# Kernel optimization log

Hardware: AMD Instinct MI355X
Metric: run time of the kernel (lower is better)

The kernel has to match this reference:

```python
import jax, jax.numpy as jnp
import numpy as np

B, T, X_DIM, Y_DIM, H_DIM = 16, 1000, 8, 4, 48
GAMMA = 1e-4
ITERS = 200


def setup_inputs() -> dict:
    key = jax.random.key(0)
    ks = jax.random.split(key, 20)
    def rn(i, shape, s=1.0):
        return jax.random.normal(ks[i], shape, dtype=jnp.float32) * jnp.float32(s)
    E = 2 * H_DIM + X_DIM  # edge-MLP input width = [h, h_nbr, message]
    s_e = float(1.0 / np.sqrt(E))
    s_h = float(1.0 / np.sqrt(H_DIM))
    A = rn(4, (X_DIM, X_DIM), 0.1)
    Bm = rn(5, (Y_DIM, Y_DIM), 0.1)
    z = lambda n: jnp.zeros((n,), jnp.float32)
    return dict(
        ys=rn(0, (B, T, Y_DIM)),
        hx0=rn(1, (B, H_DIM, T)),
        F_mat=jnp.eye(X_DIM, dtype=jnp.float32) + rn(2, (X_DIM, X_DIM), 0.05),
        H_mat=rn(3, (Y_DIM, X_DIM), 0.3),
        Q=A @ A.T + 0.5 * jnp.eye(X_DIM, dtype=jnp.float32),  # SPD process noise
        R=Bm @ Bm.T + 0.5 * jnp.eye(Y_DIM, dtype=jnp.float32),  # SPD obs noise
        W_hy=rn(6, (H_DIM, Y_DIM), 0.5), b_hy=z(H_DIM),
        W1_past=rn(7, (H_DIM, E), s_e), b1_past=z(H_DIM),
        W2_past=rn(8, (H_DIM, H_DIM), s_h), b2_past=z(H_DIM),
        W1_fut=rn(9, (H_DIM, E), s_e), b1_fut=z(H_DIM),
        W2_fut=rn(10, (H_DIM, H_DIM), s_h), b2_fut=z(H_DIM),
        W1_y=rn(11, (H_DIM, E), s_e), b1_y=z(H_DIM),
        W2_y=rn(12, (H_DIM, H_DIM), s_h), b2_y=z(H_DIM),
        W_ih=rn(13, (3 * H_DIM, H_DIM), s_h), b_ih=z(3 * H_DIM),
        W_hh=rn(14, (3 * H_DIM, H_DIM), s_h), b_hh=z(3 * H_DIM),
        W_dec=rn(15, (X_DIM, H_DIM), s_h), b_dec=z(X_DIM),
        iterations=ITERS,
    )


def reference(ys, hx0, F_mat, H_mat, Q, R, W_hy, b_hy,
              W1_past, b1_past, W2_past, b2_past,
              W1_fut, b1_fut, W2_fut, b2_fut,
              W1_y, b1_y, W2_y, b2_y,
              W_ih, b_ih, W_hh, b_hh, W_dec, b_dec, iterations):
    Qi = jnp.linalg.inv(Q)
    Ri = jnp.linalg.inv(R)
    ysT = jnp.swapaxes(ys, 1, 2)                      # (B, y_dim, T)
    xs0 = jnp.einsum('yx,byt->bxt', H_mat, ysT)       # H^T y init  (B, x_dim, T)
    hy = jnp.einsum('hy,byt->bht', W_hy, ysT) + b_hy[None, :, None]
    Tn = ys.shape[1]
    not_first = (jnp.arange(Tn) > 0).astype(ys.dtype)        # mask t=0
    not_last = (jnp.arange(Tn) < Tn - 1).astype(ys.dtype)    # mask t=T-1

    def messages(xs):
        x_past = jnp.pad(xs[:, :, :-1], ((0, 0), (0, 0), (1, 0)))
        x_fut = jnp.pad(xs[:, :, 1:], ((0, 0), (0, 0), (0, 1)))
        mp = -jnp.einsum('ij,bjt->bit', Qi, xs - jnp.einsum('ij,bjt->bit', F_mat, x_past)) * not_first
        mf = jnp.einsum('ji,jk,bkt->bit', F_mat, Qi, x_fut - jnp.einsum('jk,bkt->bjt', F_mat, xs)) * not_last
        my = jnp.einsum('yi,yz,bzt->bit', H_mat, Ri, ysT - jnp.einsum('yx,bxt->byt', H_mat, xs))
        return mp, mf, my

    def edge(h, hn, m, W1, b1, W2, b2):
        inp = jnp.concatenate([h, hn, m], axis=1)     # (B, 2h+x_dim, T)
        mid = jax.nn.relu(jnp.einsum('oi,bit->bot', W1, inp) + b1[None, :, None])
        return jnp.einsum('oi,bit->bot', W2, mid) + b2[None, :, None]

    def gnn(hx, mp, mf, my):
        h_past = jnp.pad(hx[:, :, :-1], ((0, 0), (0, 0), (1, 0)))
        h_fut = jnp.pad(hx[:, :, 1:], ((0, 0), (0, 0), (0, 1)))
        agg = (edge(hx, h_past, mp, W1_past, b1_past, W2_past, b2_past)
               + edge(hx, h_fut, mf, W1_fut, b1_fut, W2_fut, b2_fut)
               + edge(hx, hy, my, W1_y, b1_y, W2_y, b2_y))
        gx = jnp.einsum('oi,bit->bot', W_ih, agg) + b_ih[None, :, None]
        gh = jnp.einsum('oi,bit->bot', W_hh, hx) + b_hh[None, :, None]
        xr, xz, xn = jnp.split(gx, 3, axis=1)
        hr, hz, hn = jnp.split(gh, 3, axis=1)
        r = jax.nn.sigmoid(xr + hr)
        zg = jax.nn.sigmoid(xz + hz)
        n = jnp.tanh(xn + r * hn)
        hx_new = (1.0 - zg) * n + zg * hx
        eps = jnp.einsum('oi,bit->bot', W_dec, hx_new) + b_dec[None, :, None]
        return eps, hx_new

    def step(carry, _):
        xs, hx = carry
        mp, mf, my = messages(xs)
        eps, hx = gnn(hx, mp, mf, my)
        xs = xs + jnp.float32(GAMMA) * (eps + mp + mf + my)
        return (xs, hx), xs

    (xs, hx), iter_preds = jax.lax.scan(step, (xs0, hx0), None, length=iterations)
    return xs, iter_preds  # (B,x_dim,T), (iterations,B,x_dim,T)
```

## Files before the change

### kernel.cpp

```cpp
#include <hip/hip_runtime.h>
#include <math.h>

#define T_DIM 1000
#define BB    16
#define XD    8
#define YD    4
#define HD    48
#define NITER 200
#define GAMMA 1e-4f

#define HALO  25
#define FUSE  25
#define NLNCH 8
#define SC    128
#define EFF   (SC - 2*HALO)
#define NTI   13
#define HP    56

typedef __attribute__((ext_vector_type(8))) short bf16x8;
typedef __attribute__((ext_vector_type(4))) float f32x4;
typedef __attribute__((ext_vector_type(2))) float f32x2;
typedef __attribute__((ext_vector_type(4))) unsigned short us4;
typedef __attribute__((ext_vector_type(2))) unsigned u32x2;
typedef __attribute__((ext_vector_type(4))) unsigned u32x4;

#define MFMA16(a,b,c) __builtin_amdgcn_mfma_f32_16x16x32_bf16((a),(b),(c),0,0,0)

__device__ inline unsigned short f2b(float x) {
  union { float f; unsigned u; } v; v.f = x;
  unsigned r = (v.u + 0x7FFFu + ((v.u >> 16) & 1u)) >> 16;
  return (unsigned short)r;
}
__device__ inline bf16x8 ldg8(const unsigned short* p) { return *(const bf16x8*)p; }
__device__ inline unsigned pk2(float a, float b) {
  return (unsigned)f2b(a) | ((unsigned)f2b(b) << 16);
}
__device__ inline bf16x8 mk8(unsigned a, unsigned b, unsigned c, unsigned d) {
  union { u32x4 u; bf16x8 v; } t; t.u[0]=a; t.u[1]=b; t.u[2]=c; t.u[3]=d; return t.v;
}
__device__ inline void qswap(unsigned x0, unsigned x1, unsigned &A, unsigned &B) {
  u32x2 s = __builtin_amdgcn_permlane32_swap(x0, x1, false, false);
  u32x2 t = __builtin_amdgcn_permlane16_swap(s[0], s[1], false, false);
  A = t[0]; B = t[1];
}
__device__ inline void frag48(const f32x4 m0, const f32x4 m1, const f32x4 m2,
                              int quad, bf16x8 &c0, bf16x8 &c1) {
  unsigned p00 = pk2(m0[0], m0[1]), p01 = pk2(m0[2], m0[3]);
  unsigned p10 = pk2(m1[0], m1[1]), p11 = pk2(m1[2], m1[3]);
  unsigned p20 = pk2(m2[0], m2[1]), p21 = pk2(m2[2], m2[3]);
  unsigned A0,B0,A1,B1,A2,B2,A3,B3;
  qswap(p00, p10, A0, B0);
  qswap(p01, p11, A1, B1);
  qswap(p20, p20, A2, B2);
  qswap(p21, p21, A3, B3);
  c0 = mk8(A0, A1, B0, B1);
  unsigned t0, t1, t2, t3;
  if (quad < 2)       { t0 = A2; t1 = A3; t2 = B2; t3 = B3; }
  else if (quad == 2) { t0 = 0x3F80u; t1 = 0; t2 = 0; t3 = 0; }
  else                { t0 = 0; t1 = 0; t2 = 0; t3 = 0; }
  c1 = mk8(t0, t1, t2, t3);
}

__global__ __launch_bounds__(64) void precompute_mats_kernel(
    const float* __restrict__ F, const float* __restrict__ Hm,
    const float* __restrict__ Q, const float* __restrict__ R,
    float* __restrict__ mats)
{
  __shared__ float sQi[64], sRi[16], sF[64], sH[32], sFtQi[64], sHtRi[32];
  const int t = threadIdx.x;
  if (t < 64) sF[t] = F[t];
  if (t < 32) sH[t] = Hm[t];
  {
    float col[8];
    #pragma unroll
    for (int i = 0; i < 8; i++)
      col[i] = (t < 8) ? Q[i*8 + t] : ((t < 16 && i == t - 8) ? 1.f : 0.f);
    #pragma unroll
    for (int c = 0; c < 8; c++) {
      float Mcc = __shfl(col[c], c);
      float f[8];
      #pragma unroll
      for (int r = 0; r < 8; r++) f[r] = __shfl(col[r], c);
      float newc = col[c] / Mcc;
      col[c] = newc;
      #pragma unroll
      for (int r = 0; r < 8; r++) if (r != c) col[r] -= f[r] * newc;
    }
    if (t >= 8 && t < 16) {
      #pragma unroll
      for (int i = 0; i < 8; i++) sQi[i*8 + (t - 8)] = col[i];
    }
  }
  {
    float col[4];
    #pragma unroll
    for (int i = 0; i < 4; i++)
      col[i] = (t < 4) ? R[i*4 + t] : ((t < 8 && i == t - 4) ? 1.f : 0.f);
    #pragma unroll
    for (int c = 0; c < 4; c++) {
      float Mcc = __shfl(col[c], c);
      float f[4];
      #pragma unroll
      for (int r = 0; r < 4; r++) f[r] = __shfl(col[r], c);
      float newc = col[c] / Mcc;
      col[c] = newc;
      #pragma unroll
      for (int r = 0; r < 4; r++) if (r != c) col[r] -= f[r] * newc;
    }
    if (t >= 4 && t < 8) {
      #pragma unroll
      for (int i = 0; i < 4; i++) sRi[i*4 + (t - 4)] = col[i];
    }
  }
  __syncthreads();
  const int i = t >> 3, j = t & 7;
  mats[t] = sQi[t];
  { float s = 0.f; for (int k = 0; k < 8; k++) s += sQi[i*8+k] * sF[k*8+j]; mats[64 + t] = s; }
  { float s = 0.f; for (int k = 0; k < 8; k++) s += sF[k*8+i] * sQi[k*8+j]; mats[128 + t] = s; sFtQi[t] = s; }
  if (t < 32) {
    int ii = t >> 2, z = t & 3;
    float s = 0.f; for (int y = 0; y < 4; y++) s += sH[y*8+ii] * sRi[y*4+z];
    mats[256 + t] = s; sHtRi[t] = s;
  }
  __syncthreads();
  { float s = 0.f; for (int k = 0; k < 8; k++) s += sFtQi[i*8+k] * sF[k*8+j]; mats[192 + t] = s; }
  { float s = 0.f; for (int z = 0; z < 4; z++) s += sHtRi[i*4+z] * sH[z*8+j]; mats[288 + t] = s; }
}

__global__ void precompute_bt_kernel(const float* __restrict__ ys,
                                     const float* __restrict__ W_hy, const float* __restrict__ b_hy,
                                     const float* __restrict__ Hm, const float* __restrict__ mats,
                                     unsigned short* __restrict__ hy_b,
                                     float* __restrict__ mconst, float* __restrict__ xs0)
{
  int idx = blockIdx.x * 256 + threadIdx.x;
  if (idx >= BB * T_DIM) return;
  int b = idx / T_DIM, t = idx - b * T_DIM;
  float yy[YD];
  #pragma unroll
  for (int y = 0; y < YD; y++) yy[y] = ys[(b*T_DIM + t)*YD + y];
  #pragma unroll 4
  for (int h = 0; h < HD; h++) {
    float s = b_hy[h];
    #pragma unroll
    for (int y = 0; y < YD; y++) s += W_hy[h*YD+y] * yy[y];
    hy_b[(b*T_DIM + t)*HD + h] = f2b(s);
  }
  const float* HtRi = mats + 256;
  #pragma unroll
  for (int x = 0; x < XD; x++) {
    float s0 = 0.f, s1 = 0.f;
    #pragma unroll
    for (int y = 0; y < YD; y++) {
      s0 += Hm[y*XD + x] * yy[y];
      s1 += HtRi[x*YD + y] * yy[y];
    }
    xs0[(b*XD + x)*T_DIM + t]    = s0;
    mconst[(b*XD + x)*T_DIM + t] = s1;
  }
}

struct WP {
  const float *W1[3], *b1[3], *W2[3], *b2[3], *Wih, *bih, *Whh, *bhh, *Wdec, *bdec;
  unsigned short *W1b, *W2b, *Wihb, *Whhb, *Wdecb;
};
__global__ void convert_weights_kernel(WP p) {
  int idx = blockIdx.x * 256 + threadIdx.x;
  int stride = gridDim.x * 256;
  for (int i = idx; i < 3*48*128; i += stride) {
    int e = i / (48*128), r = (i / 128) % 48, k = i & 127;
    float v = (k < 104) ? p.W1[e][r*104 + k] : (k == 104) ? p.b1[e][r] : 0.f;
    p.W1b[i] = (k <= 104) ? f2b(v) : 0;
  }
  for (int i = idx; i < 3*48*64; i += stride) {
    int e = i / (48*64), r = (i / 64) % 48, k = i & 63;
    float v = (k < HD) ? p.W2[e][r*HD + k] : (k == HD) ? p.b2[e][r] : 0.f;
    p.W2b[i] = (k <= HD) ? f2b(v) : 0;
  }
  for (int i = idx; i < 144*64; i += stride) {
    int r = i >> 6, k = i & 63;
    p.Wihb[i] = (k < HD) ? f2b(p.Wih[r*HD + k]) : (k == HD) ? f2b(p.bih[r]) : 0;
    p.Whhb[i] = (k < HD) ? f2b(p.Whh[r*HD + k]) : (k == HD) ? f2b(p.bhh[r]) : 0;
  }
  for (int i = idx; i < 16*64; i += stride) {
    int r = i >> 6, k = i & 63;
    unsigned short v = 0;
    if (r < XD) {
      if (k < HD) v = f2b(p.Wdec[r*HD + k]);
      else if (k == HD) v = f2b(p.bdec[r]);
    }
    p.Wdecb[i] = v;
  }
}

struct FP {
  const float* mats;
  const float* mconst;
  const unsigned short* hy_b;
  const unsigned short *W1b, *W2b, *Wihb, *Whhb, *Wdecb;
  const float *xs_src, *hx_src;
  float* hx_dst;
  float* out;
  int k0;
};

__global__ __launch_bounds__(512, 2)
void fused_kernel(FP P)
{
  __shared__ __align__(16) unsigned short s_hx[2][SC+2][HP];
  __shared__ __align__(16) unsigned short s_hy[SC][HD];
  __shared__ __align__(16) float s_xs[2][SC+2][12];
  __shared__ __align__(16) float s_msum[SC][8];
  __shared__ float s_mats[352];
  __shared__ __align__(16) unsigned short s_W1[3*48*128];
  __shared__ __align__(16) unsigned short s_Wih[144*64];
  __shared__ __align__(16) unsigned short s_Whh[144*64];

  const int tid  = threadIdx.x;
  const int b    = blockIdx.x / NTI;
  const int tile = blockIdx.x % NTI;
  const int goff = tile * EFF - HALO;
  const int wave = tid >> 6;
  const int lane = tid & 63;
  const int quad = lane >> 4;
  const int l16  = lane & 15;
  const int col  = wave * 16 + l16;
  const int gt   = goff + col;
  const size_t BXT = (size_t)BB * XD * T_DIM;

  const int swz = l16 & 7;
  const int ck0 = ((quad) ^ swz) * 8;
  const int ck1 = ((4 + quad) ^ swz) * 8;

  for (int i = tid; i < 352; i += 512) s_mats[i] = P.mats[i];
  for (int i = tid; i < 144*16; i += 512) {
    int r = i >> 4, c = i & 15, cs = c ^ (r & 7);
    *(bf16x8*)&s_W1[r*128 + cs*8] = *(const bf16x8*)&P.W1b[r*128 + c*8];
  }
  for (int i = tid; i < 144*8; i += 512) {
    int r = i >> 3, c = i & 7, cs = c ^ (r & 7);
    *(bf16x8*)&s_Wih[r*64 + cs*8] = *(const bf16x8*)&P.Wihb[r*64 + c*8];
    *(bf16x8*)&s_Whh[r*64 + cs*8] = *(const bf16x8*)&P.Whhb[r*64 + c*8];
  }
  for (int i = tid; i < SC*HD; i += 512) {
    int c = i / HD, h = i - c*HD, g = goff + c;
    s_hy[c][h] = (g >= 0 && g < T_DIM) ? P.hy_b[((size_t)b*T_DIM + g)*HD + h] : 0;
  }
  for (int i = tid; i < (SC+2)*HP; i += 512) {
    int c = i / HP, h = i - c*HP;
    if (c == 0 || c == SC+1) { s_hx[0][c][h] = 0; s_hx[1][c][h] = 0; }
    else if (h < HD) {
      int g = goff + c - 1;
      float v = (g >= 0 && g < T_DIM) ? P.hx_src[((size_t)b*HD + h)*T_DIM + g] : 0.f;
      s_hx[0][c][h] = f2b(v);
      s_hx[1][c][h] = 0;
    } else {
      unsigned short v = (h == HD) ? (unsigned short)0x3F80 : 0;
      s_hx[0][c][h] = v; s_hx[1][c][h] = v;
    }
  }
  for (int i = tid; i < (SC+2)*12; i += 512) {
    int c = i / 12, x = i - c*12;
    float v = 0.f;
    if (c >= 1 && c <= SC && x < XD) {
      int g = goff + c - 1;
      if (g >= 0 && g < T_DIM) v = P.xs_src[((size_t)b*XD + x)*T_DIM + g];
    }
    s_xs[0][c][x] = v;
    if (c == 0 || c == SC+1) s_xs[1][c][x] = 0.f;
  }
  float hcur[3][4];
  float mc0 = 0.f, mc1 = 0.f;
  {
    const bool v = (gt >= 0) && (gt < T_DIM);
    #pragma unroll
    for (int rt = 0; rt < 3; rt++)
      #pragma unroll
      for (int r = 0; r < 4; r++) {
        int h = rt*16 + quad*4 + r;
        hcur[rt][r] = v ? P.hx_src[((size_t)b*HD + h)*T_DIM + gt] : 0.f;
      }
    if (v) {
      mc0 = P.mconst[((size_t)b*XD + quad*2 + 0)*T_DIM + gt];
      mc1 = P.mconst[((size_t)b*XD + quad*2 + 1)*T_DIM + gt];
    }
  }
  __syncthreads();

  const bool eff = (col >= HALO) && (col < HALO + EFF);
  const bool gtv = (gt >= 0) && (gt < T_DIM);

  #pragma unroll 1
  for (int j = 0; j < FUSE; j++) {
    const int p = j & 1;
    const unsigned short (*hxP)[HP] = s_hx[p];
    unsigned short (*hxN)[HP] = s_hx[p ^ 1];
    const float (*xsP)[12] = s_xs[p];
    float (*xsN)[12] = s_xs[p ^ 1];
    const int k = P.k0 + j;
    float* out_k = P.out + BXT + (size_t)k * BXT;

    float xc[8], xp[8], xf[8];
    *(f32x4*)&xc[0] = *(const f32x4*)&xsP[col+1][0];
    *(f32x4*)&xc[4] = *(const f32x4*)&xsP[col+1][4];
    *(f32x4*)&xp[0] = *(const f32x4*)&xsP[col][0];
    *(f32x4*)&xp[4] = *(const f32x4*)&xsP[col][4];
    *(f32x4*)&xf[0] = *(const f32x4*)&xsP[col+2][0];
    *(f32x4*)&xf[4] = *(const f32x4*)&xsP[col+2][4];
    float mpv[2], mfv[2], myv[2], msv[2];
    #pragma unroll
    for (int xx = 0; xx < 2; xx++) {
      const int x = quad*2 + xx;
      float mp = 0.f, mf = 0.f, my = (xx == 0) ? mc0 : mc1;
      #pragma unroll
      for (int jj = 0; jj < 8; jj++) {
        mp += s_mats[64  + x*8 + jj] * xp[jj] - s_mats[x*8 + jj]       * xc[jj];
        mf += s_mats[128 + x*8 + jj] * xf[jj] - s_mats[192 + x*8 + jj] * xc[jj];
        my -= s_mats[288 + x*8 + jj] * xc[jj];
      }
      if (gt == 0) mp = 0.f;
      if (gt == T_DIM - 1) mf = 0.f;
      mpv[xx] = mp; mfv[xx] = mf; myv[xx] = my; msv[xx] = mp + mf + my;
    }
    { f32x2 ms; ms[0] = msv[0]; ms[1] = msv[1];
      *(f32x2*)&s_msum[col][quad*2] = ms; }

    bf16x8 b3e[3];
    #pragma unroll
    for (int e = 0; e < 3; e++) {
      unsigned d = (e == 0) ? pk2(mpv[0], mpv[1])
                 : (e == 1) ? pk2(mfv[0], mfv[1])
                            : pk2(myv[0], myv[1]);
      u32x2 s = __builtin_amdgcn_permlane32_swap(d, d, false, false);
      u32x2 a = __builtin_amdgcn_permlane16_swap(s[0], s[0], false, false);
      u32x2 g = __builtin_amdgcn_permlane16_swap(s[1], s[1], false, false);
      unsigned t0, t1, t2, t3;
      if (quad == 0)      { t0 = a[0]; t1 = a[1]; t2 = g[0]; t3 = g[1]; }
      else if (quad == 1) { t0 = 0x3F80u; t1 = 0; t2 = 0; t3 = 0; }
      else                { t0 = 0; t1 = 0; t2 = 0; t3 = 0; }
      b3e[e] = mk8(t0, t1, t2, t3);
    }

    const unsigned short* ctr = &hxP[col+1][0];
    bf16x8 ctr0 = ldg8(ctr + quad*8);
    bf16x8 ctrg = ldg8(ctr + 32 + quad*8);

    f32x4 agg[3] = {{0,0,0,0},{0,0,0,0},{0,0,0,0}};
    #pragma unroll
    for (int e = 0; e < 3; e++) {
      const unsigned short* W1e = s_W1 + e*48*128;
      const unsigned short* W2e = P.W2b + e*48*64;
      const unsigned short* nb  = (e == 0) ? &hxP[col][0]
                                : (e == 1) ? &hxP[col+2][0]
                                           : &s_hy[col][0];
      bf16x8 nbl = ldg8(nb + (quad & 1)*8);
      bf16x8 b0 = ctr0;
      bf16x8 b1 = (quad < 2) ? ctrg : nbl;
      bf16x8 b2 = ldg8(nb + 16 + quad*8);
      bf16x8 b3 = b3e[e];
      f32x4 mid[3];
      #pragma unroll
      for (int rt = 0; rt < 3; rt++) {
        const unsigned short* wr = W1e + (rt*16 + l16)*128;
        f32x4 acc = {0,0,0,0};
        acc = MFMA16(ldg8(wr + ck0),      b0, acc);
        acc = MFMA16(ldg8(wr + ck1),      b1, acc);
        acc = MFMA16(ldg8(wr + 64 + ck0), b2, acc);
        acc = MFMA16(ldg8(wr + 64 + ck1), b3, acc);
        mid[rt] = acc;
      }
      f32x4 rm0, rm1, rm2;
      #pragma unroll
      for (int r = 0; r < 4; r++) {
        rm0[r] = fmaxf(mid[0][r], 0.f);
        rm1[r] = fmaxf(mid[1][r], 0.f);
        rm2[r] = fmaxf(mid[2][r], 0.f);
      }
      bf16x8 c0, c1;
      frag48(rm0, rm1, rm2, quad, c0, c1);
      #pragma unroll
      for (int rt = 0; rt < 3; rt++) {
        const unsigned short* wr = W2e + (rt*16 + l16)*64;
        f32x4 acc = agg[rt];
        acc = MFMA16(ldg8(wr + quad*8),      c0, acc);
        acc = MFMA16(ldg8(wr + 32 + quad*8), c1, acc);
        agg[rt] = acc;
      }
    }

    bf16x8 ga0, ga1;
    frag48(agg[0], agg[1], agg[2], quad, ga0, ga1);
    bf16x8 gh0 = ctr0;
    bf16x8 gh1 = ctrg;
    f32x4 rz[6], xn[3], hn[3];
    #pragma unroll
    for (int rt = 0; rt < 6; rt++) {
      const unsigned short* wi = s_Wih + (rt*16 + l16)*64;
      const unsigned short* wh = s_Whh + (rt*16 + l16)*64;
      f32x4 acc = {0,0,0,0};
      acc = MFMA16(ldg8(wi + ck0), ga0, acc);
      acc = MFMA16(ldg8(wi + ck1), ga1, acc);
      acc = MFMA16(ldg8(wh + ck0), gh0, acc);
      acc = MFMA16(ldg8(wh + ck1), gh1, acc);
      rz[rt] = acc;
    }
    #pragma unroll
    for (int rt = 0; rt < 3; rt++) {
      const unsigned short* wi = s_Wih + ((96 + rt*16) + l16)*64;
      const unsigned short* wh = s_Whh + ((96 + rt*16) + l16)*64;
      f32x4 a1 = {0,0,0,0}, a2 = {0,0,0,0};
      a1 = MFMA16(ldg8(wi + ck0), ga0, a1);
      a1 = MFMA16(ldg8(wi + ck1), ga1, a1);
      a2 = MFMA16(ldg8(wh + ck0), gh0, a2);
      a2 = MFMA16(ldg8(wh + ck1), gh1, a2);
      xn[rt] = a1; hn[rt] = a2;
    }
    #pragma unroll
    for (int rt = 0; rt < 3; rt++) {
      us4 pk;
      #pragma unroll
      for (int r = 0; r < 4; r++) {
        float rg = 1.f / (1.f + __expf(-rz[rt][r]));
        float zg = 1.f / (1.f + __expf(-rz[3+rt][r]));
        float na = xn[rt][r] + rg * hn[rt][r];
        float e2 = __expf(2.f * na);
        float nn = 1.f - 2.f / (e2 + 1.f);
        float hnew = (1.f - zg) * nn + zg * hcur[rt][r];
        if (!gtv) hnew = 0.f;
        hcur[rt][r] = hnew;
        pk[r] = f2b(hnew);
        if (j == FUSE-1 && eff && gtv) {
          int h = rt*16 + quad*4 + r;
          P.hx_dst[((size_t)b*HD + h)*T_DIM + gt] = hnew;
        }
      }
      *(us4*)&hxN[col+1][rt*16 + quad*4] = pk;
    }

    f32x4 h0, h1, h2;
    #pragma unroll
    for (int r = 0; r < 4; r++) { h0[r] = hcur[0][r]; h1[r] = hcur[1][r]; h2[r] = hcur[2][r]; }
    bf16x8 d0, d1;
    frag48(h0, h1, h2, quad, d0, d1);
    f32x4 dec = {0,0,0,0};
    dec = MFMA16(ldg8(P.Wdecb + l16*64 + quad*8),      d0, dec);
    dec = MFMA16(ldg8(P.Wdecb + l16*64 + 32 + quad*8), d1, dec);
    if (quad < 2) {
      f32x4 msum = *(const f32x4*)&s_msum[col][quad*4];
      f32x4 xo;
      #pragma unroll
      for (int r = 0; r < 4; r++) {
        int x = quad*4 + r;
        float xnew = xsP[col+1][x] + GAMMA * (dec[r] + msum[r]);
        if (!gtv) xnew = 0.f;
        xo[r] = xnew;
        if (eff && gtv) {
          out_k[((size_t)b*XD + x)*T_DIM + gt] = xnew;
          if (k == NITER-1) P.out[((size_t)b*XD + x)*T_DIM + gt] = xnew;
        }
      }
      *(f32x4*)&xsN[col+1][quad*4] = xo;
    }

    __syncthreads();
  }
}

extern "C" void kernel_launch(void* const* d_in, const int* in_sizes, int n_in,
                              void* d_out, int out_size, void* d_ws, size_t ws_size,
                              hipStream_t stream) {
  (void)in_sizes; (void)n_in; (void)out_size; (void)ws_size;
  const float* ys  = (const float*)d_in[0];
  const float* hx0 = (const float*)d_in[1];
  const float* F   = (const float*)d_in[2];
  const float* Hm  = (const float*)d_in[3];
  const float* Q   = (const float*)d_in[4];
  const float* R   = (const float*)d_in[5];

  float* out = (float*)d_out;
  float* ws  = (float*)d_ws;

  const size_t BXT = (size_t)BB * XD * T_DIM;
  const size_t BHT = (size_t)BB * HD * T_DIM;

  float* mats   = ws;
  float* mconst = ws + 512;
  float* xs0    = mconst + BXT;
  float* hxA    = xs0 + BXT;
  float* hxB    = hxA + BHT;
  unsigned short* hy_b  = (unsigned short*)(hxB + BHT);
  unsigned short* W1b   = hy_b + BHT;
  unsigned short* W2b   = W1b + 3*48*128;
  unsigned short* Wihb  = W2b + 3*48*64;
  unsigned short* Whhb  = Wihb + 144*64;
  unsigned short* Wdecb = Whhb + 144*64;

  precompute_mats_kernel<<<1, 64, 0, stream>>>(F, Hm, Q, R, mats);
  precompute_bt_kernel<<<(BB*T_DIM + 255)/256, 256, 0, stream>>>(
      ys, (const float*)d_in[6], (const float*)d_in[7], Hm, mats, hy_b, mconst, xs0);

  WP wp;
  wp.W1[0] = (const float*)d_in[8];  wp.b1[0] = (const float*)d_in[9];
  wp.W2[0] = (const float*)d_in[10]; wp.b2[0] = (const float*)d_in[11];
  wp.W1[1] = (const float*)d_in[12]; wp.b1[1] = (const float*)d_in[13];
  wp.W2[1] = (const float*)d_in[14]; wp.b2[1] = (const float*)d_in[15];
  wp.W1[2] = (const float*)d_in[16]; wp.b1[2] = (const float*)d_in[17];
  wp.W2[2] = (const float*)d_in[18]; wp.b2[2] = (const float*)d_in[19];
  wp.Wih = (const float*)d_in[20]; wp.bih = (const float*)d_in[21];
  wp.Whh = (const float*)d_in[22]; wp.bhh = (const float*)d_in[23];
  wp.Wdec = (const float*)d_in[24]; wp.bdec = (const float*)d_in[25];
  wp.W1b = W1b; wp.W2b = W2b; wp.Wihb = Wihb; wp.Whhb = Whhb; wp.Wdecb = Wdecb;
  convert_weights_kernel<<<16, 256, 0, stream>>>(wp);

  FP P;
  P.mats = mats; P.mconst = mconst; P.hy_b = hy_b;
  P.W1b = W1b; P.W2b = W2b; P.Wihb = Wihb; P.Whhb = Whhb; P.Wdecb = Wdecb;
  P.out = out;

  for (int L = 0; L < NLNCH; L++) {
    int k0 = L * FUSE;
    P.k0 = k0;
    P.xs_src = (L == 0) ? xs0 : out + BXT + (size_t)(k0 - 1) * BXT;
    P.hx_src = (L == 0) ? hx0 : ((L & 1) ? hxA : hxB);
    P.hx_dst = (L & 1) ? hxB : hxA;
    fused_kernel<<<dim3(BB * NTI), dim3(512), 0, stream>>>(P);
  }
}
```

Baseline: 1.929 ms.

## Compute Kalman message terms with split-bf16 MFMA instead of scalar FMAs

Replaces the per-lane scalar 8x8 message matvecs (past, future, observation) with MFMA 16x16x32 bf16 products. The precomputed message matrices are stored as a block matrix in hi/lo bf16 pairs, and the xs inputs are split into hi/lo bf16 so that three MFMAs per accumulator approximate fp32 accuracy. The message sum is now redistributed through lane swaps instead of the s_msum shared-memory round trip, and the boundary masking is patched in the edge tiles only. This removes scalar FLOPs and LDS traffic from the inner loop, at the cost of a more intricate lane layout and some risk of precision loss in the xs update.

```diff
diff --git a/kernel.cpp b/kernel.cpp
--- a/kernel.cpp
+++ b/kernel.cpp
@@ -19,7 +19,6 @@
 
 typedef __attribute__((ext_vector_type(8))) short bf16x8;
 typedef __attribute__((ext_vector_type(4))) float f32x4;
-typedef __attribute__((ext_vector_type(2))) float f32x2;
 typedef __attribute__((ext_vector_type(4))) unsigned short us4;
 typedef __attribute__((ext_vector_type(2))) unsigned u32x2;
 typedef __attribute__((ext_vector_type(4))) unsigned u32x4;
@@ -30,6 +29,12 @@
   union { float f; unsigned u; } v; v.f = x;
   unsigned r = (v.u + 0x7FFFu + ((v.u >> 16) & 1u)) >> 16;
   return (unsigned short)r;
+}
+__device__ inline float b2fl(unsigned p) {
+  union { unsigned u; float f; } v; v.u = p << 16; return v.f;
+}
+__device__ inline float b2fh(unsigned p) {
+  union { unsigned u; float f; } v; v.u = p & 0xFFFF0000u; return v.f;
 }
 __device__ inline bf16x8 ldg8(const unsigned short* p) { return *(const bf16x8*)p; }
 __device__ inline unsigned pk2(float a, float b) {
@@ -64,9 +69,10 @@
 __global__ __launch_bounds__(64) void precompute_mats_kernel(
     const float* __restrict__ F, const float* __restrict__ Hm,
     const float* __restrict__ Q, const float* __restrict__ R,
-    float* __restrict__ mats)
+    float* __restrict__ mats, unsigned short* __restrict__ Mmsg)
 {
   __shared__ float sQi[64], sRi[16], sF[64], sH[32], sFtQi[64], sHtRi[32];
+  __shared__ float sQiF[64], sFtQiF[64], sHtRiH[64];
   const int t = threadIdx.x;
   if (t < 64) sF[t] = F[t];
   if (t < 32) sH[t] = Hm[t];
@@ -115,7 +121,7 @@
   __syncthreads();
   const int i = t >> 3, j = t & 7;
   mats[t] = sQi[t];
-  { float s = 0.f; for (int k = 0; k < 8; k++) s += sQi[i*8+k] * sF[k*8+j]; mats[64 + t] = s; }
+  { float s = 0.f; for (int k = 0; k < 8; k++) s += sQi[i*8+k] * sF[k*8+j]; mats[64 + t] = s; sQiF[t] = s; }
   { float s = 0.f; for (int k = 0; k < 8; k++) s += sF[k*8+i] * sQi[k*8+j]; mats[128 + t] = s; sFtQi[t] = s; }
   if (t < 32) {
     int ii = t >> 2, z = t & 3;
@@ -123,8 +129,30 @@
     mats[256 + t] = s; sHtRi[t] = s;
   }
   __syncthreads();
-  { float s = 0.f; for (int k = 0; k < 8; k++) s += sFtQi[i*8+k] * sF[k*8+j]; mats[192 + t] = s; }
-  { float s = 0.f; for (int z = 0; z < 4; z++) s += sHtRi[i*4+z] * sH[z*8+j]; mats[288 + t] = s; }
+  { float s = 0.f; for (int k = 0; k < 8; k++) s += sFtQi[i*8+k] * sF[k*8+j]; mats[192 + t] = s; sFtQiF[t] = s; }
+  { float s = 0.f; for (int z = 0; z < 4; z++) s += sHtRi[i*4+z] * sH[z*8+j]; mats[288 + t] = s; sHtRiH[t] = s; }
+  __syncthreads();
+  for (int ii = t; ii < 2048; ii += 64) {
+    int m = ii >> 9;
+    int row = (ii >> 5) & 15;
+    int kk = ii & 31;
+    int g = m >> 1, hilo = m & 1;
+    int q = row >> 2, r = row & 3, x = 2*q + (r & 1);
+    int kb = kk >> 3, jj = kk & 7;
+    float c = 0.f;
+    if (g == 0) {
+      if (r < 2) c = (kb == 0) ? sQiF[x*8+jj] : (kb >= 2) ? -sQi[x*8+jj] : 0.f;
+      else       c = (kb == 1) ? sFtQi[x*8+jj] : (kb >= 2) ? -sFtQiF[x*8+jj] : 0.f;
+    } else {
+      if (r < 2) c = (kb >= 2) ? -sHtRiH[x*8+jj] : 0.f;
+      else       c = (kb == 0) ? sQiF[x*8+jj] : (kb == 1) ? sFtQi[x*8+jj]
+                   : -(sQi[x*8+jj] + sFtQiF[x*8+jj] + sHtRiH[x*8+jj]);
+    }
+    unsigned short hv = f2b(c);
+    unsigned short out = hv;
+    if (hilo) out = f2b(c - b2fl((unsigned)hv));
+    Mmsg[(m*16 + row)*32 + ((kb ^ (row & 3)) * 8) + jj] = out;
+  }
 }
 
 __global__ void precompute_bt_kernel(const float* __restrict__ ys,
@@ -194,7 +222,7 @@
 }
 
 struct FP {
-  const float* mats;
+  const unsigned short* Mmsg;
   const float* mconst;
   const unsigned short* hy_b;
   const unsigned short *W1b, *W2b, *Wihb, *Whhb, *Wdecb;
@@ -210,8 +238,7 @@
   __shared__ __align__(16) unsigned short s_hx[2][SC+2][HP];
   __shared__ __align__(16) unsigned short s_hy[SC][HD];
   __shared__ __align__(16) float s_xs[2][SC+2][12];
-  __shared__ __align__(16) float s_msum[SC][8];
-  __shared__ float s_mats[352];
+  __shared__ __align__(16) unsigned short s_Mmsg[2048];
   __shared__ __align__(16) unsigned short s_W1[3*48*128];
   __shared__ __align__(16) unsigned short s_Wih[144*64];
   __shared__ __align__(16) unsigned short s_Whh[144*64];
@@ -231,8 +258,9 @@
   const int swz = l16 & 7;
   const int ck0 = ((quad) ^ swz) * 8;
   const int ck1 = ((4 + quad) ^ swz) * 8;
-
-  for (int i = tid; i < 352; i += 512) s_mats[i] = P.mats[i];
+  const int mck = ((quad ^ (l16 & 3)) * 8);
+
+  for (int i = tid; i < 2048; i += 512) s_Mmsg[i] = P.Mmsg[i];
   for (int i = tid; i < 144*16; i += 512) {
     int r = i >> 4, c = i & 15, cs = c ^ (r & 7);
     *(bf16x8*)&s_W1[r*128 + cs*8] = *(const bf16x8*)&P.W1b[r*128 + c*8];
@@ -289,6 +317,7 @@
 
   const bool eff = (col >= HALO) && (col < HALO + EFF);
   const bool gtv = (gt >= 0) && (gt < T_DIM);
+  const bool btile = (tile == 0) || (tile == NTI - 1);
 
   #pragma unroll 1
   for (int j = 0; j < FUSE; j++) {
@@ -300,37 +329,38 @@
     const int k = P.k0 + j;
     float* out_k = P.out + BXT + (size_t)k * BXT;
 
-    float xc[8], xp[8], xf[8];
-    *(f32x4*)&xc[0] = *(const f32x4*)&xsP[col+1][0];
-    *(f32x4*)&xc[4] = *(const f32x4*)&xsP[col+1][4];
-    *(f32x4*)&xp[0] = *(const f32x4*)&xsP[col][0];
-    *(f32x4*)&xp[4] = *(const f32x4*)&xsP[col][4];
-    *(f32x4*)&xf[0] = *(const f32x4*)&xsP[col+2][0];
-    *(f32x4*)&xf[4] = *(const f32x4*)&xsP[col+2][4];
-    float mpv[2], mfv[2], myv[2], msv[2];
-    #pragma unroll
-    for (int xx = 0; xx < 2; xx++) {
-      const int x = quad*2 + xx;
-      float mp = 0.f, mf = 0.f, my = (xx == 0) ? mc0 : mc1;
-      #pragma unroll
-      for (int jj = 0; jj < 8; jj++) {
-        mp += s_mats[64  + x*8 + jj] * xp[jj] - s_mats[x*8 + jj]       * xc[jj];
-        mf += s_mats[128 + x*8 + jj] * xf[jj] - s_mats[192 + x*8 + jj] * xc[jj];
-        my -= s_mats[288 + x*8 + jj] * xc[jj];
-      }
-      if (gt == 0) mp = 0.f;
-      if (gt == T_DIM - 1) mf = 0.f;
-      mpv[xx] = mp; mfv[xx] = mf; myv[xx] = my; msv[xx] = mp + mf + my;
-    }
-    { f32x2 ms; ms[0] = msv[0]; ms[1] = msv[1];
-      *(f32x2*)&s_msum[col][quad*2] = ms; }
+    const float* srcx = &xsP[col + ((quad == 0) ? 0 : (quad == 1) ? 2 : 1)][0];
+    f32x4 xv0 = *(const f32x4*)&srcx[0];
+    f32x4 xv1 = *(const f32x4*)&srcx[4];
+    unsigned h0 = pk2(xv0[0], xv0[1]), h1 = pk2(xv0[2], xv0[3]);
+    unsigned h2 = pk2(xv1[0], xv1[1]), h3 = pk2(xv1[2], xv1[3]);
+    unsigned l0 = pk2(xv0[0] - b2fl(h0), xv0[1] - b2fh(h0));
+    unsigned l1 = pk2(xv0[2] - b2fl(h1), xv0[3] - b2fh(h1));
+    unsigned l2 = pk2(xv1[0] - b2fl(h2), xv1[1] - b2fh(h2));
+    unsigned l3 = pk2(xv1[2] - b2fl(h3), xv1[3] - b2fh(h3));
+    bf16x8 vh = (quad == 3) ? mk8(l0, l1, l2, l3) : mk8(h0, h1, h2, h3);
+    bf16x8 vl = (quad < 2)  ? mk8(l0, l1, l2, l3) : mk8(0, 0, 0, 0);
+    bf16x8 mAh = ldg8(s_Mmsg + (0*16 + l16)*32 + mck);
+    bf16x8 mAl = ldg8(s_Mmsg + (1*16 + l16)*32 + mck);
+    bf16x8 mBh = ldg8(s_Mmsg + (2*16 + l16)*32 + mck);
+    bf16x8 mBl = ldg8(s_Mmsg + (3*16 + l16)*32 + mck);
+    f32x4 accA = {0, 0, 0, 0};
+    accA = MFMA16(mAh, vh, accA);
+    accA = MFMA16(mAl, vh, accA);
+    accA = MFMA16(mAh, vl, accA);
+    f32x4 accB = {mc0, mc1, mc0, mc1};
+    accB = MFMA16(mBh, vh, accB);
+    accB = MFMA16(mBl, vh, accB);
+    accB = MFMA16(mBh, vl, accB);
 
     bf16x8 b3e[3];
     #pragma unroll
     for (int e = 0; e < 3; e++) {
-      unsigned d = (e == 0) ? pk2(mpv[0], mpv[1])
-                 : (e == 1) ? pk2(mfv[0], mfv[1])
-                            : pk2(myv[0], myv[1]);
+      unsigned d = (e == 0) ? pk2(accA[0], accA[1])
+                 : (e == 1) ? pk2(accA[2], accA[3])
+                            : pk2(accB[0], accB[1]);
+      if (e == 0 && gt == 0) d = 0;
+      if (e == 1 && gt == T_DIM - 1) d = 0;
       u32x2 s = __builtin_amdgcn_permlane32_swap(d, d, false, false);
       u32x2 a = __builtin_amdgcn_permlane16_swap(s[0], s[0], false, false);
       u32x2 g = __builtin_amdgcn_permlane16_swap(s[1], s[1], false, false);
@@ -339,6 +369,27 @@
       else if (quad == 1) { t0 = 0x3F80u; t1 = 0; t2 = 0; t3 = 0; }
       else                { t0 = 0; t1 = 0; t2 = 0; t3 = 0; }
       b3e[e] = mk8(t0, t1, t2, t3);
+    }
+
+    unsigned mA0, mB0, mA1, mB1;
+    qswap(__float_as_uint(accB[2]), __float_as_uint(accB[3]), mA0, mB0);
+    qswap(__float_as_uint(accB[3]), __float_as_uint(accB[2]), mA1, mB1);
+    float msr0 = __uint_as_float(mA0), msr1 = __uint_as_float(mA1);
+    float msr2 = __uint_as_float(mB0), msr3 = __uint_as_float(mB1);
+    if (btile) {
+      unsigned pA0, pB0, pA1, pB1, fA0, fB0, fA1, fB1;
+      qswap(__float_as_uint(accA[0]), __float_as_uint(accA[1]), pA0, pB0);
+      qswap(__float_as_uint(accA[1]), __float_as_uint(accA[0]), pA1, pB1);
+      qswap(__float_as_uint(accA[2]), __float_as_uint(accA[3]), fA0, fB0);
+      qswap(__float_as_uint(accA[3]), __float_as_uint(accA[2]), fA1, fB1);
+      if (gt == 0) {
+        msr0 -= __uint_as_float(pA0); msr1 -= __uint_as_float(pA1);
+        msr2 -= __uint_as_float(pB0); msr3 -= __uint_as_float(pB1);
+      }
+      if (gt == T_DIM - 1) {
+        msr0 -= __uint_as_float(fA0); msr1 -= __uint_as_float(fA1);
+        msr2 -= __uint_as_float(fB0); msr3 -= __uint_as_float(fB1);
+      }
     }
 
     const unsigned short* ctr = &hxP[col+1][0];
@@ -437,21 +488,21 @@
       *(us4*)&hxN[col+1][rt*16 + quad*4] = pk;
     }
 
-    f32x4 h0, h1, h2;
-    #pragma unroll
-    for (int r = 0; r < 4; r++) { h0[r] = hcur[0][r]; h1[r] = hcur[1][r]; h2[r] = hcur[2][r]; }
+    f32x4 h0v, h1v, h2v;
+    #pragma unroll
+    for (int r = 0; r < 4; r++) { h0v[r] = hcur[0][r]; h1v[r] = hcur[1][r]; h2v[r] = hcur[2][r]; }
     bf16x8 d0, d1;
-    frag48(h0, h1, h2, quad, d0, d1);
+    frag48(h0v, h1v, h2v, quad, d0, d1);
     f32x4 dec = {0,0,0,0};
     dec = MFMA16(ldg8(P.Wdecb + l16*64 + quad*8),      d0, dec);
     dec = MFMA16(ldg8(P.Wdecb + l16*64 + 32 + quad*8), d1, dec);
     if (quad < 2) {
-      f32x4 msum = *(const f32x4*)&s_msum[col][quad*4];
+      float msr[4] = {msr0, msr1, msr2, msr3};
       f32x4 xo;
       #pragma unroll
       for (int r = 0; r < 4; r++) {
         int x = quad*4 + r;
-        float xnew = xsP[col+1][x] + GAMMA * (dec[r] + msum[r]);
+        float xnew = xsP[col+1][x] + GAMMA * (dec[r] + msr[r]);
         if (!gtv) xnew = 0.f;
         xo[r] = xnew;
         if (eff && gtv) {
@@ -484,7 +535,8 @@
   const size_t BHT = (size_t)BB * HD * T_DIM;
 
   float* mats   = ws;
-  float* mconst = ws + 512;
+  unsigned short* Mmsg = (unsigned short*)(ws + 512);
+  float* mconst = ws + 512 + 1024;
   float* xs0    = mconst + BXT;
   float* hxA    = xs0 + BXT;
   float* hxB    = hxA + BHT;
@@ -495,7 +547,7 @@
   unsigned short* Whhb  = Wihb + 144*64;
   unsigned short* Wdecb = Whhb + 144*64;
 
-  precompute_mats_kernel<<<1, 64, 0, stream>>>(F, Hm, Q, R, mats);
+  precompute_mats_kernel<<<1, 64, 0, stream>>>(F, Hm, Q, R, mats, Mmsg);
   precompute_bt_kernel<<<(BB*T_DIM + 255)/256, 256, 0, stream>>>(
       ys, (const float*)d_in[6], (const float*)d_in[7], Hm, mats, hy_b, mconst, xs0);
 
@@ -513,7 +565,7 @@
   convert_weights_kernel<<<16, 256, 0, stream>>>(wp);
 
   FP P;
-  P.mats = mats; P.mconst = mconst; P.hy_b = hy_b;
+  P.Mmsg = Mmsg; P.mconst = mconst; P.hy_b = hy_b;
   P.W1b = W1b; P.W2b = W2b; P.Wihb = Wihb; P.Whhb = Whhb; P.Wdecb = Wdecb;
   P.out = out;
 
```

New measurement: 1.939 ms. About the same (+0.5%).
